# Optimization experiments

Measured on AMD Instinct MI355X. Metric: run time of the kernel, lower is better.

## Reference

```python
import jax, jax.numpy as jnp
import numpy as np

B, C, N = 32, 1024, 256   # N=256 is hard-coded by query/key Conv1d in_channels
DQ = 256 // 4             # 64
EPS = 1e-5                # BatchNorm eps


def setup_inputs() -> dict:
    key = jax.random.key(0)
    ks = jax.random.split(key, 16)
    def bn_params(k, ch):
        k1, k2, k3, k4 = jax.random.split(k, 4)
        return (jax.random.uniform(k1, (ch,), jnp.float32, 0.5, 1.5),   # gamma
                jax.random.normal(k2, (ch,), jnp.float32) * 0.1,        # beta
                jax.random.normal(k3, (ch,), jnp.float32) * 0.1,        # running mean
                jax.random.uniform(k4, (ch,), jnp.float32, 0.5, 1.5))   # running var
    bn1 = bn_params(ks[4], DQ)
    bn2 = bn_params(ks[5], DQ)
    bn3 = bn_params(ks[6], C)
    return {
        "x": jax.random.normal(ks[0], (B, C, N), jnp.float32),
        "Wq": jax.random.normal(ks[1], (DQ, N), jnp.float32) * (1.0 / np.sqrt(N)),
        "Wk": jax.random.normal(ks[2], (DQ, N), jnp.float32) * (1.0 / np.sqrt(N)),
        "Wv": jax.random.normal(ks[3], (C, C), jnp.float32) * (1.0 / np.sqrt(C)),
        "bn1_g": bn1[0], "bn1_b": bn1[1], "bn1_m": bn1[2], "bn1_v": bn1[3],
        "bn2_g": bn2[0], "bn2_b": bn2[1], "bn2_m": bn2[2], "bn2_v": bn2[3],
        "bn3_g": bn3[0], "bn3_b": bn3[1], "bn3_m": bn3[2], "bn3_v": bn3[3],
        "alpha": jnp.full((1,), 0.1, jnp.float32),  # torch init is 0; 0.1 keeps the branch active
    }


def _bn(y, g, b, m, v):
    # eval-mode BatchNorm1d over channel axis 1 of (B, ch, L)
    scale = g / jnp.sqrt(v + EPS)
    return (y - m[None, :, None]) * scale[None, :, None] + b[None, :, None]


def reference(x, Wq, Wk, Wv,
              bn1_g, bn1_b, bn1_m, bn1_v,
              bn2_g, bn2_b, bn2_m, bn2_v,
              bn3_g, bn3_b, bn3_m, bn3_v,
              alpha):
    x_hat = jnp.swapaxes(x, 1, 2)                                   # (B, N, C)
    q = jax.nn.relu(_bn(jnp.einsum('on,bnc->boc', Wq, x_hat), bn1_g, bn1_b, bn1_m, bn1_v))  # (B, DQ, C)
    k = jax.nn.relu(_bn(jnp.einsum('on,bnc->boc', Wk, x_hat), bn2_g, bn2_b, bn2_m, bn2_v))  # (B, DQ, C)
    sim = jnp.einsum('bkc,bkd->bcd', k, q)                          # (B, C, C) channel affinity
    aff = jax.nn.softmax(jnp.max(sim, axis=-1, keepdims=True) - sim, axis=-1)
    v = jax.nn.relu(_bn(jnp.einsum('oc,bcn->bon', Wv, x), bn3_g, bn3_b, bn3_m, bn3_v))      # (B, C, N)
    out = jnp.einsum('bcd,bdn->bcn', aff, v)                        # (B, C, N)
    return alpha * out + x
```

## Files before the change

kernel.cpp:

```cpp
#include <hip/hip_runtime.h>
#include <hip/hip_bf16.h>

#define B_  32
#define C_  1024
#define N_  256
#define DQ_ 64

typedef __bf16 bf16_t;
typedef __bf16 bf16x8 __attribute__((ext_vector_type(8)));
typedef float  f32x4  __attribute__((ext_vector_type(4)));

static __device__ __forceinline__ f32x4 mfma16(bf16x8 a, bf16x8 b, f32x4 c) {
  return __builtin_amdgcn_mfma_f32_16x16x32_bf16(a, b, c, 0, 0, 0);
}

static __device__ __forceinline__ bf16x8 ldcvt(const float* p) {
  const float4 a = *(const float4*)p;
  const float4 b = *(const float4*)(p + 4);
  bf16x8 r;
  r[0] = (bf16_t)a.x; r[1] = (bf16_t)a.y; r[2] = (bf16_t)a.z; r[3] = (bf16_t)a.w;
  r[4] = (bf16_t)b.x; r[5] = (bf16_t)b.y; r[6] = (bf16_t)b.z; r[7] = (bf16_t)b.w;
  return r;
}

static __device__ __forceinline__ void stage32(const bf16_t* grow0, size_t gstride,
                                               bf16_t* tile, int wave, int lane) {
#pragma unroll
  for (int t = 0; t < 4; ++t) {
    const int rb = wave * 32 + t * 8;
    const int r  = rb + (lane >> 3);
    const int g  = ((lane & 7) - r) & 7;
    const bf16_t* src = grow0 + (size_t)r * gstride + g * 8;
    __builtin_amdgcn_global_load_lds(
        (const __attribute__((address_space(1))) void*)src,
        (__attribute__((address_space(3))) void*)(tile + rb * 64), 16, 0, 0);
  }
}

__global__ __launch_bounds__(256) void k_trans(const float* __restrict__ x,
                                               bf16_t* __restrict__ xT) {
  __shared__ bf16_t tile[32][34];
  const int b  = blockIdx.z;
  const int n0 = blockIdx.x * 32, c0 = blockIdx.y * 32;
  const int tx = threadIdx.x, ty = threadIdx.y;
  const float* xb = x + (size_t)b * C_ * N_;
  bf16_t*     xtb = xT + (size_t)b * N_ * C_;
#pragma unroll
  for (int i = 0; i < 4; ++i)
    tile[ty + i * 8][tx] = (bf16_t)xb[(size_t)(c0 + ty + i * 8) * N_ + (n0 + tx)];
  __syncthreads();
#pragma unroll
  for (int i = 0; i < 4; ++i)
    xtb[(size_t)(n0 + ty + i * 8) * C_ + (c0 + tx)] = tile[tx][ty + i * 8];
}

__global__ __launch_bounds__(256) void k_cvt(const float* __restrict__ Wv,
                                             const float* __restrict__ Wq,
                                             const float* __restrict__ Wk,
                                             bf16_t* __restrict__ Wvb,
                                             bf16_t* __restrict__ Wqkb) {
  const int gid = blockIdx.x * 256 + threadIdx.x;
  if (blockIdx.x < 512) {
    const int i = gid * 8;
    *(bf16x8*)(Wvb + i) = ldcvt(Wv + i);
  } else {
    const int g2 = (gid - 512 * 256) * 8;
    if (g2 < 16384) *(bf16x8*)(Wqkb + g2) = ldcvt(Wq + g2);
    else            *(bf16x8*)(Wqkb + g2) = ldcvt(Wk + (g2 - 16384));
  }
}

__global__ __launch_bounds__(256) void k_qk(const float* __restrict__ x,
                                            const bf16_t* __restrict__ Wqkb,
                                            const float* __restrict__ g1,
                                            const float* __restrict__ b1,
                                            const float* __restrict__ m1,
                                            const float* __restrict__ v1,
                                            const float* __restrict__ g2,
                                            const float* __restrict__ b2,
                                            const float* __restrict__ m2,
                                            const float* __restrict__ v2,
                                            bf16_t* __restrict__ qt,
                                            bf16_t* __restrict__ kt) {
  const int tid  = threadIdx.x;
  const int wave = tid >> 6;
  const int lane = tid & 63;
  const int quad = lane >> 4;
  const int l16  = lane & 15;
  const int b    = blockIdx.y;
  const int c16  = blockIdx.x * 64 + wave * 16;
  const float* xb = x + (size_t)b * C_ * N_;

  f32x4 acc[8];
#pragma unroll
  for (int i = 0; i < 8; ++i) acc[i] = (f32x4){0.f, 0.f, 0.f, 0.f};

  for (int ks = 0; ks < 8; ++ks) {
    const int k0 = ks * 32 + quad * 8;
    const bf16x8 bx = ldcvt(xb + (size_t)(c16 + l16) * N_ + k0);
#pragma unroll
    for (int i = 0; i < 8; ++i) {
      const bf16x8 aw = *(const bf16x8*)(Wqkb + (size_t)(i * 16 + l16) * N_ + k0);
      acc[i] = mfma16(aw, bx, acc[i]);
    }
  }

#pragma unroll
  for (int i = 0; i < 8; ++i) {
    const bool isq = (i < 4);
    bf16_t* dst = isq ? qt : kt;
#pragma unroll
    for (int r = 0; r < 4; ++r) {
      const int o = (i & 3) * 16 + quad * 4 + r;
      const float sc = (isq ? g1[o] : g2[o]) * rsqrtf((isq ? v1[o] : v2[o]) + 1e-5f);
      const float mm = isq ? m1[o] : m2[o];
      const float bt = isq ? b1[o] : b2[o];
      const int c = c16 + l16;
      float y = (acc[i][r] - mm) * sc + bt;
      y = fmaxf(y, 0.f);
      dst[((size_t)b * C_ + c) * DQ_ + o] = (bf16_t)y;
    }
  }
}

__global__ __launch_bounds__(256, 2) void k_vgemm(const bf16_t* __restrict__ Wvb,
                                                  const bf16_t* __restrict__ xT,
                                                  const float* __restrict__ g,
                                                  const float* __restrict__ be,
                                                  const float* __restrict__ mu,
                                                  const float* __restrict__ va,
                                                  bf16_t* __restrict__ vT) {
  __shared__ __align__(16) bf16_t As[2][128 * 64];
  __shared__ __align__(16) bf16_t Bs[2][128 * 64];
  const int tid  = threadIdx.x;
  const int wave = tid >> 6;
  const int lane = tid & 63;
  const int quad = lane >> 4;
  const int l16  = lane & 15;
  const int wid  = blockIdx.y * 8 + blockIdx.x;
  const int xcd  = wid & 7;
  const int j    = wid >> 3;
  const int o0 = (j >> 3) * 128;
  const int r0 = ((xcd << 3) | (j & 7)) * 128;
  const bf16_t* Ab = Wvb + (size_t)o0 * C_;
  const bf16_t* Bb = xT + (size_t)r0 * C_;
  const int wr = (wave >> 1) * 64, wc = (wave & 1) * 64;

  stage32(Ab, C_, (bf16_t*)As[0], wave, lane);
  stage32(Bb, C_, (bf16_t*)Bs[0], wave, lane);

  f32x4 acc[4][4];
#pragma unroll
  for (int i = 0; i < 4; ++i)
#pragma unroll
    for (int j2 = 0; j2 < 4; ++j2) acc[i][j2] = (f32x4){0.f, 0.f, 0.f, 0.f};

  for (int ks = 0; ks < 16; ++ks) {
    __syncthreads();
    const bf16_t* ca = As[ks & 1];
    const bf16_t* cb = Bs[ks & 1];
    if (ks < 15) {
      stage32(Ab + (ks + 1) * 64, C_, (bf16_t*)As[(ks + 1) & 1], wave, lane);
      stage32(Bb + (ks + 1) * 64, C_, (bf16_t*)Bs[(ks + 1) & 1], wave, lane);
    }
#pragma unroll
    for (int ksub = 0; ksub < 2; ++ksub) {
      bf16x8 a[4], bfr[4];
#pragma unroll
      for (int i = 0; i < 4; ++i) {
        const int r = wr + i * 16 + l16;
        const int s = ((ksub * 4 + quad) + r) & 7;
        a[i] = *(const bf16x8*)(ca + r * 64 + s * 8);
      }
#pragma unroll
      for (int j2 = 0; j2 < 4; ++j2) {
        const int r = wc + j2 * 16 + l16;
        const int s = ((ksub * 4 + quad) + r) & 7;
        bfr[j2] = *(const bf16x8*)(cb + r * 64 + s * 8);
      }
#pragma unroll
      for (int i = 0; i < 4; ++i)
#pragma unroll
        for (int j2 = 0; j2 < 4; ++j2)
          acc[i][j2] = mfma16(a[i], bfr[j2], acc[i][j2]);
    }
  }

#pragma unroll
  for (int i = 0; i < 4; ++i)
#pragma unroll
    for (int r = 0; r < 4; ++r) {
      const int o = o0 + wr + i * 16 + quad * 4 + r;
      const float sc = g[o] * rsqrtf(va[o] + 1e-5f);
      const float mm = mu[o], bt = be[o];
#pragma unroll
      for (int j2 = 0; j2 < 4; ++j2) {
        const int rG = r0 + wc + j2 * 16 + l16;
        float y = (acc[i][j2][r] - mm) * sc + bt;
        y = fmaxf(y, 0.f);
        vT[(size_t)rG * C_ + o] = (bf16_t)y;
      }
    }
}

static __device__ __forceinline__ int eaddr(int c, int d) {
  const int ch = d >> 3;
  const int ph = (ch & ~7) | ((ch + c) & 7);
  return (c << 10) + (ph << 3) + (d & 7);
}

__global__ __launch_bounds__(512, 2) void k_fused(const bf16_t* __restrict__ qt,
                                                  const bf16_t* __restrict__ kt,
                                                  const bf16_t* __restrict__ vT,
                                                  const float* __restrict__ x,
                                                  const float* __restrict__ alphap,
                                                  float* __restrict__ out) {
  __shared__ __align__(16) bf16_t ebuf[32 * 1024];
  __shared__ __align__(16) bf16_t vs[2][256 * 64];
  __shared__ float redmin[8][32];
  __shared__ float redsum[8][32];
  __shared__ float rowmin[32];
  __shared__ float rowrinv[32];

  const int tid  = threadIdx.x;
  const int wave = tid >> 6;
  const int lane = tid & 63;
  const int quad = lane >> 4;
  const int l16  = lane & 15;
  const int id   = blockIdx.x;
  const int b    = ((id & 7) << 2) | (id >> 8);
  const int c0   = ((id >> 3) & 31) << 5;

  const bf16_t* qb  = qt + (size_t)b * C_ * DQ_;
  const bf16_t* ktb = kt + ((size_t)b * C_ + c0) * DQ_;

  bf16x8 am[2][2];
#pragma unroll
  for (int i = 0; i < 2; ++i)
#pragma unroll
    for (int ksub = 0; ksub < 2; ++ksub)
      am[i][ksub] = *(const bf16x8*)(ktb + (size_t)(i * 16 + l16) * DQ_ + ksub * 32 + quad * 8);

  stage32(qb, DQ_, (bf16_t*)vs[0], wave, lane);
  f32x4 sim[2][8];
#pragma unroll
  for (int i = 0; i < 2; ++i)
#pragma unroll
    for (int nt = 0; nt < 8; ++nt) sim[i][nt] = (f32x4){0.f, 0.f, 0.f, 0.f};

#pragma unroll
  for (int t = 0; t < 4; ++t) {
    if (t < 3) {
      stage32(qb + (size_t)(t + 1) * 256 * DQ_, DQ_, (bf16_t*)vs[(t + 1) & 1], wave, lane);
      asm volatile("s_waitcnt vmcnt(4)" ::: "memory");
    } else {
      asm volatile("s_waitcnt vmcnt(0)" ::: "memory");
    }
    const bf16_t* cur = vs[t & 1];
#pragma unroll
    for (int jn = 0; jn < 2; ++jn) {
      const int r = wave * 32 + jn * 16 + l16;
#pragma unroll
      for (int ksub = 0; ksub < 2; ++ksub) {
        const int s = ((ksub * 4 + quad) + r) & 7;
        const bf16x8 bq = *(const bf16x8*)(cur + r * 64 + s * 8);
        sim[0][t * 2 + jn] = mfma16(am[0][ksub], bq, sim[0][t * 2 + jn]);
        sim[1][t * 2 + jn] = mfma16(am[1][ksub], bq, sim[1][t * 2 + jn]);
      }
    }
  }

  const bf16_t* vb = vT + (size_t)b * N_ * C_;
  stage32(vb, C_, (bf16_t*)vs[0], wave, lane);

  float pmin[2][4];
#pragma unroll
  for (int i = 0; i < 2; ++i)
#pragma unroll
    for (int r = 0; r < 4; ++r) pmin[i][r] = sim[i][0][r];
#pragma unroll
  for (int nt = 1; nt < 8; ++nt)
#pragma unroll
    for (int i = 0; i < 2; ++i)
#pragma unroll
      for (int r = 0; r < 4; ++r) pmin[i][r] = fminf(pmin[i][r], sim[i][nt][r]);
#pragma unroll
  for (int m = 1; m < 16; m <<= 1)
#pragma unroll
    for (int i = 0; i < 2; ++i)
#pragma unroll
      for (int r = 0; r < 4; ++r) pmin[i][r] = fminf(pmin[i][r], __shfl_xor(pmin[i][r], m));
  if (l16 == 0)
#pragma unroll
    for (int i = 0; i < 2; ++i)
#pragma unroll
      for (int r = 0; r < 4; ++r) redmin[wave][i * 16 + quad * 4 + r] = pmin[i][r];
  __syncthreads();
  if (tid < 32) {
    float v = redmin[0][tid];
#pragma unroll
    for (int w = 1; w < 8; ++w) v = fminf(v, redmin[w][tid]);
    rowmin[tid] = v;
  }
  __syncthreads();

  float mn[2][4], psum[2][4];
#pragma unroll
  for (int i = 0; i < 2; ++i)
#pragma unroll
    for (int r = 0; r < 4; ++r) {
      mn[i][r] = rowmin[i * 16 + quad * 4 + r];
      psum[i][r] = 0.f;
    }
#pragma unroll
  for (int nt = 0; nt < 8; ++nt) {
    const int d = ((nt >> 1) << 8) + wave * 32 + ((nt & 1) << 4) + l16;
#pragma unroll
    for (int i = 0; i < 2; ++i)
#pragma unroll
      for (int r = 0; r < 4; ++r) {
        const int c = i * 16 + quad * 4 + r;
        const float e = __expf(mn[i][r] - sim[i][nt][r]);
        ebuf[eaddr(c, d)] = (bf16_t)e;
        psum[i][r] += e;
      }
  }
#pragma unroll
  for (int m = 1; m < 16; m <<= 1)
#pragma unroll
    for (int i = 0; i < 2; ++i)
#pragma unroll
      for (int r = 0; r < 4; ++r) psum[i][r] += __shfl_xor(psum[i][r], m);
  if (l16 == 0)
#pragma unroll
    for (int i = 0; i < 2; ++i)
#pragma unroll
      for (int r = 0; r < 4; ++r) redsum[wave][i * 16 + quad * 4 + r] = psum[i][r];
  __syncthreads();
  if (tid < 32) {
    float s = redsum[0][tid];
#pragma unroll
    for (int w = 1; w < 8; ++w) s += redsum[w][tid];
    rowrinv[tid] = 1.f / s;
  }
  __syncthreads();

  f32x4 oacc[2][2];
#pragma unroll
  for (int i = 0; i < 2; ++i)
#pragma unroll
    for (int jn = 0; jn < 2; ++jn) oacc[i][jn] = (f32x4){0.f, 0.f, 0.f, 0.f};

#pragma unroll
  for (int ks = 0; ks < 16; ++ks) {
    if (ks < 15) {
      stage32(vb + (ks + 1) * 64, C_, (bf16_t*)vs[(ks + 1) & 1], wave, lane);
      asm volatile("s_waitcnt vmcnt(4)" ::: "memory");
    } else {
      asm volatile("s_waitcnt vmcnt(0)" ::: "memory");
    }
    const bf16_t* cur = vs[ks & 1];
#pragma unroll
    for (int ksub = 0; ksub < 2; ++ksub) {
      const int gch = ks * 8 + ksub * 4 + quad;
      const int ph  = (gch & ~7) | ((gch + l16) & 7);
      const bf16x8 ae0 = *(const bf16x8*)(ebuf + ((size_t)l16 << 10) + ph * 8);
      const bf16x8 ae1 = *(const bf16x8*)(ebuf + ((size_t)(16 + l16) << 10) + ph * 8);
#pragma unroll
      for (int jn = 0; jn < 2; ++jn) {
        const int r = wave * 32 + jn * 16 + l16;
        const int s = ((ksub * 4 + quad) + r) & 7;
        const bf16x8 bv = *(const bf16x8*)(cur + r * 64 + s * 8);
        oacc[0][jn] = mfma16(ae0, bv, oacc[0][jn]);
        oacc[1][jn] = mfma16(ae1, bv, oacc[1][jn]);
      }
    }
  }

  const float alpha = alphap[0];
#pragma unroll
  for (int i = 0; i < 2; ++i)
#pragma unroll
    for (int jn = 0; jn < 2; ++jn)
#pragma unroll
      for (int r = 0; r < 4; ++r) {
        const int c = c0 + i * 16 + quad * 4 + r;
        const int n = wave * 32 + jn * 16 + l16;
        const size_t idx = ((size_t)b * C_ + c) * N_ + n;
        out[idx] = alpha * (oacc[i][jn][r] * rowrinv[i * 16 + quad * 4 + r]) + x[idx];
      }
}

extern "C" void kernel_launch(void* const* d_in, const int* in_sizes, int n_in,
                              void* d_out, int out_size, void* d_ws, size_t ws_size,
                              hipStream_t stream) {
  const float* x    = (const float*)d_in[0];
  const float* Wq   = (const float*)d_in[1];
  const float* Wk   = (const float*)d_in[2];
  const float* Wv   = (const float*)d_in[3];
  const float* bn1g = (const float*)d_in[4];
  const float* bn1b = (const float*)d_in[5];
  const float* bn1m = (const float*)d_in[6];
  const float* bn1v = (const float*)d_in[7];
  const float* bn2g = (const float*)d_in[8];
  const float* bn2b = (const float*)d_in[9];
  const float* bn2m = (const float*)d_in[10];
  const float* bn2v = (const float*)d_in[11];
  const float* bn3g = (const float*)d_in[12];
  const float* bn3b = (const float*)d_in[13];
  const float* bn3m = (const float*)d_in[14];
  const float* bn3v = (const float*)d_in[15];
  const float* alph = (const float*)d_in[16];
  float* outp = (float*)d_out;

  char* ws = (char*)d_ws;
  bf16_t* qt   = (bf16_t*)(ws);
  bf16_t* kt   = (bf16_t*)(ws + (size_t)(4u << 20));
  bf16_t* vT   = (bf16_t*)(ws + (size_t)(8u << 20));
  bf16_t* xT   = (bf16_t*)(ws + (size_t)(24u << 20));
  bf16_t* Wvb  = (bf16_t*)(ws + (size_t)(40u << 20));
  bf16_t* Wqkb = (bf16_t*)(ws + (size_t)(42u << 20));

  k_trans<<<dim3(8, 32, 32), dim3(32, 8, 1), 0, stream>>>(x, xT);
  k_cvt<<<dim3(528), 256, 0, stream>>>(Wv, Wq, Wk, Wvb, Wqkb);
  k_qk<<<dim3(16, 32), 256, 0, stream>>>(x, Wqkb,
                                         bn1g, bn1b, bn1m, bn1v,
                                         bn2g, bn2b, bn2m, bn2v, qt, kt);
  k_vgemm<<<dim3(8, 64), 256, 0, stream>>>(Wvb, xT, bn3g, bn3b, bn3m, bn3v, vT);
  k_fused<<<dim3(1024), 512, 0, stream>>>(qt, kt, vT, x, alph, outp);
}
```

Before: 232.3 us.

## Fuse x transpose into QK projection kernel and vectorize q/k stores

Removes the separate transpose kernel. The QK projection kernel now stages its bf16-converted x tile in shared memory and writes the transposed xT slice itself, so x is read from global memory once instead of twice. It also precomputes BatchNorm scale and shift into shared memory and writes q/k as 4-wide vectors instead of scalar stores. The trade-offs are higher LDS use per block (~34KB) and an extra barrier in the QK kernel.

Result: faster. 227.4 us (median of 2 runs) (-2.1%).

```diff
diff --git a/kernel.cpp b/kernel.cpp
--- a/kernel.cpp
+++ b/kernel.cpp
@@ -7,6 +7,7 @@
 #define DQ_ 64
 
 typedef __bf16 bf16_t;
+typedef __bf16 bf16x4 __attribute__((ext_vector_type(4)));
 typedef __bf16 bf16x8 __attribute__((ext_vector_type(8)));
 typedef float  f32x4  __attribute__((ext_vector_type(4)));
 
@@ -35,23 +36,6 @@
         (const __attribute__((address_space(1))) void*)src,
         (__attribute__((address_space(3))) void*)(tile + rb * 64), 16, 0, 0);
   }
-}
-
-__global__ __launch_bounds__(256) void k_trans(const float* __restrict__ x,
-                                               bf16_t* __restrict__ xT) {
-  __shared__ bf16_t tile[32][34];
-  const int b  = blockIdx.z;
-  const int n0 = blockIdx.x * 32, c0 = blockIdx.y * 32;
-  const int tx = threadIdx.x, ty = threadIdx.y;
-  const float* xb = x + (size_t)b * C_ * N_;
-  bf16_t*     xtb = xT + (size_t)b * N_ * C_;
-#pragma unroll
-  for (int i = 0; i < 4; ++i)
-    tile[ty + i * 8][tx] = (bf16_t)xb[(size_t)(c0 + ty + i * 8) * N_ + (n0 + tx)];
-  __syncthreads();
-#pragma unroll
-  for (int i = 0; i < 4; ++i)
-    xtb[(size_t)(n0 + ty + i * 8) * C_ + (c0 + tx)] = tile[tx][ty + i * 8];
 }
 
 __global__ __launch_bounds__(256) void k_cvt(const float* __restrict__ Wv,
@@ -70,18 +54,21 @@
   }
 }
 
-__global__ __launch_bounds__(256) void k_qk(const float* __restrict__ x,
-                                            const bf16_t* __restrict__ Wqkb,
-                                            const float* __restrict__ g1,
-                                            const float* __restrict__ b1,
-                                            const float* __restrict__ m1,
-                                            const float* __restrict__ v1,
-                                            const float* __restrict__ g2,
-                                            const float* __restrict__ b2,
-                                            const float* __restrict__ m2,
-                                            const float* __restrict__ v2,
-                                            bf16_t* __restrict__ qt,
-                                            bf16_t* __restrict__ kt) {
+__global__ __launch_bounds__(256) void k_qkt(const float* __restrict__ x,
+                                             const bf16_t* __restrict__ Wqkb,
+                                             const float* __restrict__ g1,
+                                             const float* __restrict__ b1,
+                                             const float* __restrict__ m1,
+                                             const float* __restrict__ v1,
+                                             const float* __restrict__ g2,
+                                             const float* __restrict__ b2,
+                                             const float* __restrict__ m2,
+                                             const float* __restrict__ v2,
+                                             bf16_t* __restrict__ qt,
+                                             bf16_t* __restrict__ kt,
+                                             bf16_t* __restrict__ xT) {
+  __shared__ __align__(16) bf16_t txp[64][264];
+  __shared__ float bnsc[128], bnsh[128];
   const int tid  = threadIdx.x;
   const int wave = tid >> 6;
   const int lane = tid & 63;
@@ -89,7 +76,16 @@
   const int l16  = lane & 15;
   const int b    = blockIdx.y;
   const int c16  = blockIdx.x * 64 + wave * 16;
+  const int cl   = wave * 16 + l16;
   const float* xb = x + (size_t)b * C_ * N_;
+
+  if (tid < 128) {
+    const int o = tid & 63;
+    const bool isq = tid < 64;
+    const float sc = (isq ? g1[o] : g2[o]) * rsqrtf((isq ? v1[o] : v2[o]) + 1e-5f);
+    bnsc[tid] = sc;
+    bnsh[tid] = (isq ? b1[o] : b2[o]) - (isq ? m1[o] : m2[o]) * sc;
+  }
 
   f32x4 acc[8];
 #pragma unroll
@@ -98,28 +94,41 @@
   for (int ks = 0; ks < 8; ++ks) {
     const int k0 = ks * 32 + quad * 8;
     const bf16x8 bx = ldcvt(xb + (size_t)(c16 + l16) * N_ + k0);
+    *(bf16x8*)(&txp[cl][k0]) = bx;
 #pragma unroll
     for (int i = 0; i < 8; ++i) {
       const bf16x8 aw = *(const bf16x8*)(Wqkb + (size_t)(i * 16 + l16) * N_ + k0);
       acc[i] = mfma16(aw, bx, acc[i]);
     }
   }
-
+  __syncthreads();
+
+  {
+    bf16_t* xtb = xT + (size_t)b * N_ * C_ + (size_t)tid * C_ + blockIdx.x * 64;
+#pragma unroll
+    for (int cc = 0; cc < 8; ++cc) {
+      bf16x8 o8;
+#pragma unroll
+      for (int j = 0; j < 8; ++j) o8[j] = txp[cc * 8 + j][tid];
+      *(bf16x8*)(xtb + cc * 8) = o8;
+    }
+  }
+
+  const int c = c16 + l16;
 #pragma unroll
   for (int i = 0; i < 8; ++i) {
     const bool isq = (i < 4);
     bf16_t* dst = isq ? qt : kt;
+    const int o0  = (i & 3) * 16 + quad * 4;
+    const int bno = (isq ? 0 : 64) + o0;
+    bf16x4 w;
 #pragma unroll
     for (int r = 0; r < 4; ++r) {
-      const int o = (i & 3) * 16 + quad * 4 + r;
-      const float sc = (isq ? g1[o] : g2[o]) * rsqrtf((isq ? v1[o] : v2[o]) + 1e-5f);
-      const float mm = isq ? m1[o] : m2[o];
-      const float bt = isq ? b1[o] : b2[o];
-      const int c = c16 + l16;
-      float y = (acc[i][r] - mm) * sc + bt;
+      float y = acc[i][r] * bnsc[bno + r] + bnsh[bno + r];
       y = fmaxf(y, 0.f);
-      dst[((size_t)b * C_ + c) * DQ_ + o] = (bf16_t)y;
-    }
+      w[r] = (bf16_t)y;
+    }
+    *(bf16x4*)(dst + ((size_t)b * C_ + c) * DQ_ + o0) = w;
   }
 }
 
@@ -421,11 +430,10 @@
   bf16_t* Wvb  = (bf16_t*)(ws + (size_t)(40u << 20));
   bf16_t* Wqkb = (bf16_t*)(ws + (size_t)(42u << 20));
 
-  k_trans<<<dim3(8, 32, 32), dim3(32, 8, 1), 0, stream>>>(x, xT);
   k_cvt<<<dim3(528), 256, 0, stream>>>(Wv, Wq, Wk, Wvb, Wqkb);
-  k_qk<<<dim3(16, 32), 256, 0, stream>>>(x, Wqkb,
-                                         bn1g, bn1b, bn1m, bn1v,
-                                         bn2g, bn2b, bn2m, bn2v, qt, kt);
+  k_qkt<<<dim3(16, 32), 256, 0, stream>>>(x, Wqkb,
+                                          bn1g, bn1b, bn1m, bn1v,
+                                          bn2g, bn2b, bn2m, bn2v, qt, kt, xT);
   k_vgemm<<<dim3(8, 64), 256, 0, stream>>>(Wvb, xT, bn3g, bn3b, bn3m, bn3v, vT);
   k_fused<<<dim3(1024), 512, 0, stream>>>(qt, kt, vT, x, alph, outp);
 }
```
